# Kernel tuning notes

Hardware: AMD Instinct MI355X
Metric: run time of the kernel (lower is better)

Reference implementation:

```python
import jax, jax.numpy as jnp
import numpy as np

INPUT_DIM, DK, DV = 1024, 128, 128


def setup_inputs() -> dict:
    key = jax.random.key(0)
    ks = jax.random.split(key, 7)
    s = 0.02
    return {
        "x": jax.random.normal(ks[0], (4, 4096, INPUT_DIM), dtype=jnp.float32),
        "Wq": jax.random.normal(ks[1], (INPUT_DIM, DK), dtype=jnp.float32) * s,
        "bq": jnp.zeros((DK,), dtype=jnp.float32),
        "Wk": jax.random.normal(ks[2], (INPUT_DIM, DK), dtype=jnp.float32) * s,
        "bk": jnp.zeros((DK,), dtype=jnp.float32),
        "Wv": jax.random.normal(ks[3], (INPUT_DIM, DV), dtype=jnp.float32) * s,
        "bv": jnp.zeros((DV,), dtype=jnp.float32),
    }


def reference(x, Wq, bq, Wk, bk, Wv, bv):
    # single-head self-attention with explicit QK^T softmax V
    scale = DK ** (-0.5)
    q = x @ Wq + bq          # [b, s, dk]
    k = x @ Wk + bk          # [b, s, dk]
    v = x @ Wv + bv          # [b, s, dv]
    scores = jnp.einsum("bqd,bkd->bqk", q, k) * scale  # [b, s, s]
    attn = jax.nn.softmax(scores, axis=-1)
    return jnp.einsum("bqk,bkd->bqd", attn, v)  # [b, s, dv]
```

## Files before the change

kernel.cpp:

```cpp
#include <hip/hip_runtime.h>
#include <hip/hip_bf16.h>
#include <math.h>
#include <stdint.h>


#define SM_SCALE2 0.1275310225216245f

using f32x4  = __attribute__((ext_vector_type(4))) float;
using f32x16 = __attribute__((ext_vector_type(16))) float;
using bf16x8 = __attribute__((ext_vector_type(8))) short;
using s16x4  = __attribute__((ext_vector_type(4))) short;

#define GLD16(gp, lp) __builtin_amdgcn_global_load_lds(                      \
    (const __attribute__((address_space(1))) void*)(gp),                     \
    (__attribute__((address_space(3))) void*)(lp), 16, 0, 0)

__device__ __forceinline__ short f2bf(float f) {
  union { __hip_bfloat16 h; short s; } u;
  u.h = __float2bfloat16(f);
  return u.s;
}

__global__ __launch_bounds__(256) void wprep_k(const float* __restrict__ Wq,
                                               const float* __restrict__ Wk,
                                               const float* __restrict__ Wv,
                                               short* __restrict__ Wt) {
  int tid = blockIdx.x * 256 + threadIdx.x;
  int mat = tid >> 17;
  int r   = tid & 131071;
  int k   = r >> 7;
  int col = r & 127;
  const float* W = (mat == 0) ? Wq : ((mat == 1) ? Wk : Wv);
  const int T = k >> 6, kc = (k >> 5) & 1, g = (k >> 3) & 3, e = k & 7;
  const int cg = col >> 4, l = col & 15;
  Wt[((((mat * 16 + T) * 2 + kc) * 8 + cg) << 9) + ((g * 16 + l) << 3) + e] =
      f2bf(W[k * 128 + col]);
}

__global__ __launch_bounds__(256) void proj_k(const float* __restrict__ x,
                                              const short* __restrict__ Wt,
                                              const float* __restrict__ bq,
                                              const float* __restrict__ bk,
                                              const float* __restrict__ bv,
                                              short* __restrict__ Qb,
                                              short* __restrict__ Kb,
                                              short* __restrict__ Vt) {
  const int r0  = blockIdx.x * 64;
  const int tid  = threadIdx.x;
  const int lane = tid & 63;
  const int w    = tid >> 6;
  const int g    = lane >> 4;
  const int l15  = lane & 15;

  __shared__ __align__(16) char smem[18432];
  const char* Wtb = (const char*)Wt;

  f32x4 acc[3][4][2];
  #pragma unroll
  for (int m = 0; m < 3; ++m)
    #pragma unroll
    for (int rb = 0; rb < 4; ++rb)
      #pragma unroll
      for (int cb = 0; cb < 2; ++cb) acc[m][rb][cb] = (f32x4){0.f, 0.f, 0.f, 0.f};

  const int xrow = tid >> 2;
  const int xsl  = tid & 3;

#define XS(B) (smem + (B) * 8192)

#define BARX do {                                                             \
    __builtin_amdgcn_sched_barrier(0);                                        \
    asm volatile("s_waitcnt lgkmcnt(0)" ::: "memory");                        \
    __builtin_amdgcn_s_barrier();                                             \
    __builtin_amdgcn_sched_barrier(0);                                        \
  } while (0)

#define LOADW(DST, T) do {                                                    \
    _Pragma("unroll")                                                         \
    for (int i = 0; i < 12; ++i) {                                            \
      const int m_ = i >> 2, cb_ = (i >> 1) & 1, kc_ = i & 1;                 \
      DST[i] = *(const bf16x8*)(Wtb +                                         \
          ((((((m_ * 16 + (T)) * 2 + kc_) * 8) + (w * 2 + cb_)) << 10) +      \
           (lane << 4)));                                                     \
    }                                                                         \
  } while (0)

#define LOADX(FX, T) do {                                                     \
    _Pragma("unroll")                                                         \
    for (int p = 0; p < 4; ++p) {                                             \
      const int s = xsl + 4 * p;                                              \
      FX[p] = *(const float4*)(x + (size_t)(r0 + xrow) * 1024 + (T) * 64 + s * 4); \
    }                                                                         \
  } while (0)

#define WRITEX(B, FX) do {                                                    \
    char* xb_ = XS(B);                                                        \
    _Pragma("unroll")                                                         \
    for (int p = 0; p < 4; ++p) {                                             \
      const int s = xsl + 4 * p;                                              \
      s16x4 h = { f2bf(FX[p].x), f2bf(FX[p].y), f2bf(FX[p].z), f2bf(FX[p].w) }; \
      *(s16x4*)(xb_ + xrow * 128 + (((s >> 1) ^ (xrow & 7)) << 4) +           \
                ((s & 1) << 3)) = h;                                          \
    }                                                                         \
  } while (0)

#define COMP(B, WF) do {                                                      \
    const char* xb = XS(B);                                                   \
    _Pragma("unroll")                                                         \
    for (int kc = 0; kc < 2; ++kc) {                                          \
      bf16x8 a[4];                                                            \
      _Pragma("unroll")                                                       \
      for (int rb = 0; rb < 4; ++rb)                                          \
        a[rb] = *(const bf16x8*)(xb + (rb * 16 + l15) * 128 +                 \
                                 ((((kc << 2) + g) ^ (l15 & 7)) << 4));       \
      _Pragma("unroll")                                                       \
      for (int m = 0; m < 3; ++m)                                             \
        _Pragma("unroll")                                                     \
        for (int cb = 0; cb < 2; ++cb)                                        \
          _Pragma("unroll")                                                   \
          for (int rb = 0; rb < 4; ++rb)                                      \
            acc[m][rb][cb] = __builtin_amdgcn_mfma_f32_16x16x32_bf16(         \
                a[rb], WF[m * 4 + cb * 2 + kc], acc[m][rb][cb], 0, 0, 0);     \
    }                                                                         \
  } while (0)

  bf16x8 wf[12];
  float4 fxA[4], fxB[4];

  {
    float4 fx0[4];
    LOADX(fx0, 0);
    WRITEX(0, fx0);
    LOADW(wf, 0);
    LOADX(fxA, 1);
  }
  BARX;

  #pragma unroll 1
  for (int t = 0; t < 16; t += 2) {
    if (t + 2 < 16) LOADX(fxB, t + 2);
    COMP(0, wf);
    LOADW(wf, t + 1);
    WRITEX(1, fxA);
    BARX;
    if (t + 3 < 16) LOADX(fxA, t + 3);
    COMP(1, wf);
    if (t + 2 < 16) {
      LOADW(wf, t + 2);
      WRITEX(0, fxB);
    }
    BARX;
  }
#undef LOADW
#undef LOADX
#undef WRITEX
#undef COMP
#undef BARX
#undef XS

  #pragma unroll
  for (int m = 0; m < 2; ++m) {
    short* dst = (m == 0) ? Qb : Kb;
    const float* bias = (m == 0) ? bq : bk;
    #pragma unroll
    for (int cb = 0; cb < 2; ++cb) {
      const int col = w * 32 + cb * 16 + l15;
      const float bc = bias[col];
      #pragma unroll
      for (int rb = 0; rb < 4; ++rb)
        #pragma unroll
        for (int r = 0; r < 4; ++r) {
          float v = acc[m][rb][cb][r] + bc;
          if (m == 0) v *= SM_SCALE2;
          dst[(size_t)(r0 + rb * 16 + (g << 2) + r) * 128 + col] = f2bf(v);
        }
    }
  }
  __syncthreads();
  {
    short* tb = (short*)smem;
    #pragma unroll
    for (int cb = 0; cb < 2; ++cb) {
      const int col = w * 32 + cb * 16 + l15;
      const float bc = bv[col];
      #pragma unroll
      for (int rb = 0; rb < 4; ++rb)
        #pragma unroll
        for (int r = 0; r < 4; ++r)
          tb[col * 72 + rb * 16 + (g << 2) + r] = f2bf(acc[2][rb][cb][r] + bc);
    }
    __syncthreads();
    const int bb = r0 >> 12;
    const int s0 = r0 & 4095;
    const int d  = tid >> 1;
    #pragma unroll
    for (int j = 0; j < 4; ++j) {
      uint4 vd = *(const uint4*)((char*)tb + d * 144 + (tid & 1) * 64 + j * 16);
      *(uint4*)((char*)Vt +
                ((size_t)(bb * 128 + d) * 4096 + s0 + (tid & 1) * 32 + j * 8) * 2) = vd;
    }
  }
}

__global__ __launch_bounds__(256, 2) void attn_part_k(
    const short* __restrict__ Qb, const short* __restrict__ Kb,
    const short* __restrict__ Vt, float* __restrict__ part,
    float2* __restrict__ ml, float* __restrict__ out, int ns, int direct) {
  const int nwg  = gridDim.x;
  const int bid  = blockIdx.x;
  const int orig = (bid & 7) * (nwg >> 3) + (bid >> 3);
  const int split = orig >> 7;
  const int qb    = orig & 127;
  const int nkt   = 64 / ns;
  const int kt0   = split * nkt;

  const int tid  = threadIdx.x;
  const int lane = tid & 63;
  const int w    = tid >> 6;
  const int l31  = lane & 31;
  const bool hi  = lane >= 32;

  __shared__ __align__(16) char smem[65536];

  const int bb = qb >> 5;
  const size_t qg = (size_t)qb * 128 + w * 32 + l31;

  const char* Kg = (const char*)(Kb + ((size_t)bb << 19));
  const char* Vg = (const char*)(Vt + ((size_t)bb << 19));

  bf16x8 qf[8];
  {
    const short* qp = Qb + qg * 128;
    #pragma unroll
    for (int kd = 0; kd < 8; ++kd)
      qf[kd] = *(const bf16x8*)(qp + 16 * kd + (hi ? 8 : 0));
  }

  float m = -__builtin_inff(), lsum = 0.f;
  f32x16 oacc[4];
  #pragma unroll
  for (int dt = 0; dt < 4; ++dt) oacc[dt] = (f32x16)(0.0f);

#define STAGE(BUF, KT) do {                                                   \
    char* kb_ = smem + (BUF) * 32768;                                         \
    char* vb_ = kb_ + 16384;                                                  \
    _Pragma("unroll")                                                         \
    for (int c = 0; c < 4; ++c) {                                             \
      const int o   = w * 4096 + c * 1024 + lane * 16;                        \
      const int kr  = o >> 8;                                                 \
      const int kc_ = (o >> 4) & 15;                                          \
      GLD16(Kg + (size_t)((KT) * 64 + kr) * 256 + ((kc_ ^ (kr & 15)) << 4),   \
            kb_ + w * 4096 + c * 1024);                                       \
      const int dr  = o >> 7;                                                 \
      const int dc_ = (o >> 4) & 7;                                           \
      GLD16(Vg + (size_t)dr * 8192 + (size_t)(KT) * 128 + ((dc_ ^ (dr & 7)) << 4), \
            vb_ + w * 4096 + c * 1024);                                       \
    }                                                                         \
  } while (0)

  STAGE(0, kt0);
  __syncthreads();

  for (int t = 0; t < nkt; ++t) {
    const int cur = t & 1;
    if (t + 1 < nkt) STAGE(cur ^ 1, kt0 + t + 1);

    const char* KT_ = smem + cur * 32768;
    const char* VT_ = KT_ + 16384;

    f32x16 s0 = (f32x16)(0.0f), s1 = (f32x16)(0.0f);
    __builtin_amdgcn_s_setprio(1);
    #pragma unroll
    for (int kd = 0; kd < 8; ++kd) {
      const int ch = (((2 * kd + (hi ? 1 : 0)) ^ (l31 & 15)) << 4);
      bf16x8 k0 = *(const bf16x8*)(KT_ + l31 * 256 + ch);
      bf16x8 k1 = *(const bf16x8*)(KT_ + (32 + l31) * 256 + ch);
      s0 = __builtin_amdgcn_mfma_f32_32x32x16_bf16(k0, qf[kd], s0, 0, 0, 0);
      s1 = __builtin_amdgcn_mfma_f32_32x32x16_bf16(k1, qf[kd], s1, 0, 0, 0);
    }
    __builtin_amdgcn_s_setprio(0);

    float mx = s0[0];
    #pragma unroll
    for (int i = 1; i < 16; ++i) mx = fmaxf(mx, s0[i]);
    #pragma unroll
    for (int i = 0; i < 16; ++i) mx = fmaxf(mx, s1[i]);
    mx = fmaxf(mx, __shfl_xor(mx, 32));
    if (!__all(mx - m <= 8.f)) {
      const float mn = fmaxf(m, mx);
      const float al = exp2f(m - mn);
      m = mn;
      lsum *= al;
      #pragma unroll
      for (int dt = 0; dt < 4; ++dt)
        #pragma unroll
        for (int i = 0; i < 16; ++i) oacc[dt][i] *= al;
    }
    float rs = 0.f;
    #pragma unroll
    for (int i = 0; i < 16; ++i) { s0[i] = exp2f(s0[i] - m); rs += s0[i]; }
    #pragma unroll
    for (int i = 0; i < 16; ++i) { s1[i] = exp2f(s1[i] - m); rs += s1[i]; }
    rs += __shfl_xor(rs, 32);
    lsum += rs;

    unsigned int W[2][4][2];
    #pragma unroll
    for (int rho = 0; rho < 4; ++rho)
      #pragma unroll
      for (int rh = 0; rh < 2; ++rh) {
        asm("v_cvt_pk_bf16_f32 %0, %1, %2"
            : "=v"(W[0][rho][rh]) : "v"(s0[4 * rho + 2 * rh]), "v"(s0[4 * rho + 2 * rh + 1]));
        asm("v_cvt_pk_bf16_f32 %0, %1, %2"
            : "=v"(W[1][rho][rh]) : "v"(s1[4 * rho + 2 * rh]), "v"(s1[4 * rho + 2 * rh + 1]));
      }

    #pragma unroll
    for (int ks = 0; ks < 4; ++ks) {
      const int t2 = ks >> 1, ksl = ks & 1;
      const unsigned int wl0 = W[t2][2 * ksl][0],     wl1 = W[t2][2 * ksl][1];
      const unsigned int wh0 = W[t2][2 * ksl + 1][0], wh1 = W[t2][2 * ksl + 1][1];
      const unsigned int r0 = __shfl_xor(hi ? wl0 : wh0, 32);
      const unsigned int r1 = __shfl_xor(hi ? wl1 : wh1, 32);
      union { unsigned int u[4]; bf16x8 v; } pb;
      pb.u[0] = hi ? r0 : wl0;
      pb.u[1] = hi ? r1 : wl1;
      pb.u[2] = hi ? wh0 : r0;
      pb.u[3] = hi ? wh1 : r1;
      __builtin_amdgcn_s_setprio(1);
      #pragma unroll
      for (int dt = 0; dt < 4; ++dt) {
        const int row = 32 * dt + l31;
        bf16x8 vf = *(const bf16x8*)(VT_ + row * 128 +
                                     (((2 * ks + (hi ? 1 : 0)) ^ (row & 7)) << 4));
        oacc[dt] = __builtin_amdgcn_mfma_f32_32x32x16_bf16(vf, pb.v, oacc[dt], 0, 0, 0);
      }
      __builtin_amdgcn_s_setprio(0);
    }

    __syncthreads();
  }
#undef STAGE

  const float sc = direct ? (1.f / lsum) : 1.f;
  float* dst = direct ? (out + qg * 128)
                      : (part + ((size_t)split * 16384 + qg) * 128);
  #pragma unroll
  for (int dt = 0; dt < 4; ++dt)
    #pragma unroll
    for (int rq = 0; rq < 4; ++rq) {
      f32x4 v = { oacc[dt][4 * rq + 0] * sc, oacc[dt][4 * rq + 1] * sc,
                  oacc[dt][4 * rq + 2] * sc, oacc[dt][4 * rq + 3] * sc };
      *(f32x4*)(dst + dt * 32 + rq * 8 + (hi ? 4 : 0)) = v;
    }
  if (!direct && lane < 32)
    ml[(size_t)split * 16384 + qg] = make_float2(m, lsum);
}

__global__ __launch_bounds__(256) void merge_k(const float* __restrict__ part,
                                               const float2* __restrict__ ml,
                                               float* __restrict__ out, int ns) {
  const int idx = blockIdx.x * 256 + threadIdx.x;
  const int row = idx >> 5;
  const int c4  = idx & 31;

  float M = -__builtin_inff();
  for (int s = 0; s < ns; ++s) M = fmaxf(M, ml[s * 16384 + row].x);
  float L = 0.f;
  for (int s = 0; s < ns; ++s) {
    const float2 v = ml[s * 16384 + row];
    L += v.y * exp2f(v.x - M);
  }
  const float invL = 1.f / L;

  f32x4 o = (f32x4){0.f, 0.f, 0.f, 0.f};
  for (int s = 0; s < ns; ++s) {
    const float wgt = exp2f(ml[s * 16384 + row].x - M) * invL;
    const f32x4 a = *(const f32x4*)(part + ((size_t)s * 16384 + row) * 128 + c4 * 4);
    o += a * wgt;
  }
  *(f32x4*)(out + (size_t)row * 128 + c4 * 4) = o;
}

extern "C" void kernel_launch(void* const* d_in, const int* in_sizes, int n_in,
                              void* d_out, int out_size, void* d_ws, size_t ws_size,
                              hipStream_t stream) {
  (void)in_sizes; (void)n_in; (void)out_size;
  const float* x  = (const float*)d_in[0];
  const float* Wq = (const float*)d_in[1];
  const float* bq = (const float*)d_in[2];
  const float* Wk = (const float*)d_in[3];
  const float* bk = (const float*)d_in[4];
  const float* Wv = (const float*)d_in[5];
  const float* bv = (const float*)d_in[6];
  float* out = (float*)d_out;

  char* ws = (char*)d_ws;
  short* Wt = (short*)ws;
  short* Qb = (short*)(ws + 786432);
  short* Kb = (short*)(ws + 786432 + 4194304);
  short* Vt = (short*)(ws + 786432 + 2 * 4194304);
  const size_t base = 786432 + 3ull * 4194304;

  const size_t per_split = 16384ull * 128 * 4 + 16384ull * 8;
  int ns = 0;
  if (ws_size >= base + 4 * per_split)      ns = 4;
  else if (ws_size >= base + 2 * per_split) ns = 2;
  const int direct = (ns == 0);
  if (direct) ns = 1;

  float*  part = (float*)(ws + base);
  float2* mlp  = (float2*)(ws + base + (size_t)ns * 16384ull * 128 * 4);

  wprep_k<<<dim3(1536), dim3(256), 0, stream>>>(Wq, Wk, Wv, Wt);
  proj_k<<<dim3(256), dim3(256), 0, stream>>>(x, Wt, bq, bk, bv, Qb, Kb, Vt);
  attn_part_k<<<dim3(128 * ns), dim3(256), 0, stream>>>(Qb, Kb, Vt, part, mlp, out,
                                                        ns, direct);
  if (!direct)
    merge_k<<<dim3(2048), dim3(256), 0, stream>>>(part, mlp, out, ns);
}
```

Before: 94.46 us.

## Split projection work across 8 waves per block instead of 4

The projection kernel now launches 512 threads per block. Each of 8 waves computes 3 of the 24 output column groups (Q, K and V, 16 columns each) instead of 6, which halves per-thread accumulators, weight fragments and x loads. The goal is more waves per CU for latency hiding and less register pressure in the projection phase. In exchange, more waves share the same LDS x tile, so each x fragment is read from LDS by more waves, and barriers cover more waves.

```diff
diff --git a/kernel.cpp b/kernel.cpp
--- a/kernel.cpp
+++ b/kernel.cpp
@@ -37,7 +37,7 @@
       f2bf(W[k * 128 + col]);
 }
 
-__global__ __launch_bounds__(256) void proj_k(const float* __restrict__ x,
+__global__ __launch_bounds__(512) void proj_k(const float* __restrict__ x,
                                               const short* __restrict__ Wt,
                                               const float* __restrict__ bq,
                                               const float* __restrict__ bk,
@@ -55,16 +55,14 @@
   __shared__ __align__(16) char smem[18432];
   const char* Wtb = (const char*)Wt;
 
-  f32x4 acc[3][4][2];
+  f32x4 acc[3][4];
   #pragma unroll
-  for (int m = 0; m < 3; ++m)
-    #pragma unroll
-    for (int rb = 0; rb < 4; ++rb)
-      #pragma unroll
-      for (int cb = 0; cb < 2; ++cb) acc[m][rb][cb] = (f32x4){0.f, 0.f, 0.f, 0.f};
-
-  const int xrow = tid >> 2;
-  const int xsl  = tid & 3;
+  for (int fi = 0; fi < 3; ++fi)
+    #pragma unroll
+    for (int rb = 0; rb < 4; ++rb) acc[fi][rb] = (f32x4){0.f, 0.f, 0.f, 0.f};
+
+  const int xrow = tid >> 3;
+  const int xsl  = tid & 7;
 
 #define XS(B) (smem + (B) * 8192)
 
@@ -77,18 +75,20 @@
 
 #define LOADW(DST, T) do {                                                    \
     _Pragma("unroll")                                                         \
-    for (int i = 0; i < 12; ++i) {                                            \
-      const int m_ = i >> 2, cb_ = (i >> 1) & 1, kc_ = i & 1;                 \
+    for (int i = 0; i < 6; ++i) {                                             \
+      const int fi_ = i >> 1, kc_ = i & 1;                                    \
+      const int f_  = w * 3 + fi_;                                            \
+      const int m_  = f_ >> 3, cg_ = f_ & 7;                                  \
       DST[i] = *(const bf16x8*)(Wtb +                                         \
-          ((((((m_ * 16 + (T)) * 2 + kc_) * 8) + (w * 2 + cb_)) << 10) +      \
+          ((((((m_ * 16 + (T)) * 2 + kc_) * 8) + cg_) << 10) +                \
            (lane << 4)));                                                     \
     }                                                                         \
   } while (0)
 
 #define LOADX(FX, T) do {                                                     \
     _Pragma("unroll")                                                         \
-    for (int p = 0; p < 4; ++p) {                                             \
-      const int s = xsl + 4 * p;                                              \
+    for (int p = 0; p < 2; ++p) {                                             \
+      const int s = xsl + 8 * p;                                              \
       FX[p] = *(const float4*)(x + (size_t)(r0 + xrow) * 1024 + (T) * 64 + s * 4); \
     }                                                                         \
   } while (0)
@@ -96,8 +96,8 @@
 #define WRITEX(B, FX) do {                                                    \
     char* xb_ = XS(B);                                                        \
     _Pragma("unroll")                                                         \
-    for (int p = 0; p < 4; ++p) {                                             \
-      const int s = xsl + 4 * p;                                              \
+    for (int p = 0; p < 2; ++p) {                                             \
+      const int s = xsl + 8 * p;                                              \
       s16x4 h = { f2bf(FX[p].x), f2bf(FX[p].y), f2bf(FX[p].z), f2bf(FX[p].w) }; \
       *(s16x4*)(xb_ + xrow * 128 + (((s >> 1) ^ (xrow & 7)) << 4) +           \
                 ((s & 1) << 3)) = h;                                          \
@@ -114,21 +114,19 @@
         a[rb] = *(const bf16x8*)(xb + (rb * 16 + l15) * 128 +                 \
                                  ((((kc << 2) + g) ^ (l15 & 7)) << 4));       \
       _Pragma("unroll")                                                       \
-      for (int m = 0; m < 3; ++m)                                             \
+      for (int fi = 0; fi < 3; ++fi)                                          \
         _Pragma("unroll")                                                     \
-        for (int cb = 0; cb < 2; ++cb)                                        \
-          _Pragma("unroll")                                                   \
-          for (int rb = 0; rb < 4; ++rb)                                      \
-            acc[m][rb][cb] = __builtin_amdgcn_mfma_f32_16x16x32_bf16(         \
-                a[rb], WF[m * 4 + cb * 2 + kc], acc[m][rb][cb], 0, 0, 0);     \
+        for (int rb = 0; rb < 4; ++rb)                                        \
+          acc[fi][rb] = __builtin_amdgcn_mfma_f32_16x16x32_bf16(              \
+              a[rb], WF[fi * 2 + kc], acc[fi][rb], 0, 0, 0);                  \
     }                                                                         \
   } while (0)
 
-  bf16x8 wf[12];
-  float4 fxA[4], fxB[4];
+  bf16x8 wf[6];
+  float4 fxA[2], fxB[2];
 
   {
-    float4 fx0[4];
+    float4 fx0[2];
     LOADX(fx0, 0);
     WRITEX(0, fx0);
     LOADW(wf, 0);
@@ -159,19 +157,20 @@
 #undef XS
 
   #pragma unroll
-  for (int m = 0; m < 2; ++m) {
-    short* dst = (m == 0) ? Qb : Kb;
-    const float* bias = (m == 0) ? bq : bk;
-    #pragma unroll
-    for (int cb = 0; cb < 2; ++cb) {
-      const int col = w * 32 + cb * 16 + l15;
-      const float bc = bias[col];
+  for (int fi = 0; fi < 3; ++fi) {
+    const int f   = w * 3 + fi;
+    const int m_  = f >> 3;
+    const int cg_ = f & 7;
+    const int col = cg_ * 16 + l15;
+    if (m_ < 2) {
+      short* dst = (m_ == 0) ? Qb : Kb;
+      const float bc = ((m_ == 0) ? bq : bk)[col];
       #pragma unroll
       for (int rb = 0; rb < 4; ++rb)
         #pragma unroll
         for (int r = 0; r < 4; ++r) {
-          float v = acc[m][rb][cb][r] + bc;
-          if (m == 0) v *= SM_SCALE2;
+          float v = acc[fi][rb][r] + bc;
+          if (m_ == 0) v *= SM_SCALE2;
           dst[(size_t)(r0 + rb * 16 + (g << 2) + r) * 128 + col] = f2bf(v);
         }
     }
@@ -180,24 +179,27 @@
   {
     short* tb = (short*)smem;
     #pragma unroll
-    for (int cb = 0; cb < 2; ++cb) {
-      const int col = w * 32 + cb * 16 + l15;
-      const float bc = bv[col];
-      #pragma unroll
-      for (int rb = 0; rb < 4; ++rb)
+    for (int fi = 0; fi < 3; ++fi) {
+      const int f = w * 3 + fi;
+      if ((f >> 3) == 2) {
+        const int col = (f & 7) * 16 + l15;
+        const float bc = bv[col];
         #pragma unroll
-        for (int r = 0; r < 4; ++r)
-          tb[col * 72 + rb * 16 + (g << 2) + r] = f2bf(acc[2][rb][cb][r] + bc);
+        for (int rb = 0; rb < 4; ++rb)
+          #pragma unroll
+          for (int r = 0; r < 4; ++r)
+            tb[col * 72 + rb * 16 + (g << 2) + r] = f2bf(acc[fi][rb][r] + bc);
+      }
     }
     __syncthreads();
     const int bb = r0 >> 12;
     const int s0 = r0 & 4095;
-    const int d  = tid >> 1;
-    #pragma unroll
-    for (int j = 0; j < 4; ++j) {
-      uint4 vd = *(const uint4*)((char*)tb + d * 144 + (tid & 1) * 64 + j * 16);
+    const int d  = tid >> 2;
+    #pragma unroll
+    for (int j = 0; j < 2; ++j) {
+      uint4 vd = *(const uint4*)((char*)tb + d * 144 + (tid & 3) * 32 + j * 16);
       *(uint4*)((char*)Vt +
-                ((size_t)(bb * 128 + d) * 4096 + s0 + (tid & 1) * 32 + j * 8) * 2) = vd;
+                ((size_t)(bb * 128 + d) * 4096 + s0 + (tid & 3) * 16 + j * 8) * 2) = vd;
     }
   }
 }
@@ -413,7 +415,7 @@
   float2* mlp  = (float2*)(ws + base + (size_t)ns * 16384ull * 128 * 4);
 
   wprep_k<<<dim3(1536), dim3(256), 0, stream>>>(Wq, Wk, Wv, Wt);
-  proj_k<<<dim3(256), dim3(256), 0, stream>>>(x, Wt, bq, bk, bv, Qb, Kb, Vt);
+  proj_k<<<dim3(256), dim3(512), 0, stream>>>(x, Wt, bq, bk, bv, Qb, Kb, Vt);
   attn_part_k<<<dim3(128 * ns), dim3(256), 0, stream>>>(Qb, Kb, Vt, part, mlp, out,
                                                         ns, direct);
   if (!direct)
```

Result: no change. 93.57 us (-0.9%).
